# Performance work log

Measured on AMD Instinct MI355X. Metric: run time of the kernel, lower is better.

The kernel has to match this reference:

```python
import jax, jax.numpy as jnp
import numpy as np

D = 4          # simulated tensor-parallel devices (shard_axis size)
B, S = 2, 4096 # batch, seq_len
DIN_S = 512    # per-device input feature shard (full d_model = D*DIN_S = 2048)
DOUT_S = 2048  # per-device output feature shard (full d_out = D*DOUT_S = 8192)


def setup_inputs() -> dict:
    key = jax.random.key(0)
    kx, kw, kb = jax.random.split(key, 3)
    x = jax.random.normal(kx, (D, B, S, DIN_S), dtype=jnp.float32)
    # lecun_normal-style scale: std = 1/sqrt(fan_in) with fan_in = full input dim
    W = jax.random.normal(kw, (D, D, DIN_S, DOUT_S), dtype=jnp.float32) / np.sqrt(D * DIN_S)
    b = jax.random.normal(kb, (D, DOUT_S), dtype=jnp.float32) * 0.01
    return {"x": x, "W": W, "b": b}


def reference(x, W, b):
    # 'gather' TP strategy: device d gathers all input shards x_i and computes
    #   y_d = sum_i x_i @ W[d, i] + b[d]   (bias only added once, by shard idx==0)
    # x: [D, B, S, DIN_S], W: [D_out_dev, D_in_shard, DIN_S, DOUT_S], b: [D, DOUT_S]
    y = jnp.einsum('ibsk,diko->dbso', x, W)  # sum over gathered shards i and k
    return y + b[:, None, None, :]
```

## Files before the change

### kernel.cpp

```cpp
#include <hip/hip_runtime.h>
#include <hip/hip_bf16.h>

#define D_   4
#define M_   8192
#define K_   2048
#define N_   2048
#define DIN  512

typedef __attribute__((ext_vector_type(8))) short  short8v;
typedef __attribute__((ext_vector_type(4))) float  f32x4;

__device__ __forceinline__ unsigned short f2bf(float f) {
  union { float f; unsigned int u; } v; v.f = f;
  unsigned int u = v.u;
  return (unsigned short)((u + 0x7fffu + ((u >> 16) & 1u)) >> 16);
}

__global__ __launch_bounds__(256) void convert_x_kernel(const float* __restrict__ x,
                                                        unsigned short* __restrict__ A) {
  unsigned int tid = blockIdx.x * 256u + threadIdx.x;
  unsigned int kg  = tid & 63u;
  unsigned int i   = (tid >> 6) & 3u;
  unsigned int m   = tid >> 8;
  const float4* src = (const float4*)(x + (size_t)i * ((size_t)M_ * DIN)
                                        + (size_t)m * DIN + (size_t)kg * 8);
  float4 a = src[0];
  float4 b = src[1];
  uint4 pk;
  pk.x = (unsigned int)f2bf(a.x) | ((unsigned int)f2bf(a.y) << 16);
  pk.y = (unsigned int)f2bf(a.z) | ((unsigned int)f2bf(a.w) << 16);
  pk.z = (unsigned int)f2bf(b.x) | ((unsigned int)f2bf(b.y) << 16);
  pk.w = (unsigned int)f2bf(b.z) | ((unsigned int)f2bf(b.w) << 16);
  *(uint4*)(A + (size_t)tid * 8) = pk;
}

__global__ __launch_bounds__(256) void transpose_w_kernel(const float* __restrict__ W,
                                                          unsigned short* __restrict__ Wt) {
  __shared__ float tile[64][65];
  const int d  = blockIdx.z;
  const int k0 = blockIdx.x * 64;
  const int o0 = blockIdx.y * 64;
  const int t  = threadIdx.x;
  const float* src = W + (size_t)d * ((size_t)K_ * N_) + (size_t)k0 * N_ + o0;
  const int c4 = (t & 15) * 4;
  const int r  = t >> 4;
  #pragma unroll
  for (int j = 0; j < 64; j += 16) {
    float4 v = *(const float4*)(src + (size_t)(r + j) * N_ + c4);
    tile[r + j][c4 + 0] = v.x; tile[r + j][c4 + 1] = v.y;
    tile[r + j][c4 + 2] = v.z; tile[r + j][c4 + 3] = v.w;
  }
  __syncthreads();
  unsigned short* dst = Wt + (size_t)d * ((size_t)N_ * K_);
  const int kk = (t & 7) * 8;
  const int oo = t >> 3;
  #pragma unroll
  for (int p = 0; p < 64; p += 32) {
    const int o = oo + p;
    unsigned short tmp[8];
    #pragma unroll
    for (int i = 0; i < 8; i++) tmp[i] = f2bf(tile[kk + i][o]);
    *(uint4*)(dst + (size_t)(o0 + o) * K_ + k0 + kk) = *(uint4*)tmp;
  }
}

#define GLL16(gp, lp)                                                              \
  __builtin_amdgcn_global_load_lds(                                               \
      (const __attribute__((address_space(1))) void*)(gp),                        \
      (__attribute__((address_space(3))) void*)(lp), 16, 0, 0)

#define NT_ 64

__global__ __launch_bounds__(512, 2) void gemm_kernel(const unsigned short* __restrict__ A,
                                                      const unsigned short* __restrict__ Bt,
                                                      const float* __restrict__ bias,
                                                      float* __restrict__ C) {
  __shared__ __align__(16) unsigned short sT[4 * 16384];
  const int tid  = threadIdx.x;
  const int w    = tid >> 6;
  const int lane = tid & 63;
  const int d    = blockIdx.z;

  const int lin     = blockIdx.y * 8 + blockIdx.x;
  const int tile_id = (lin & 7) * 32 + (lin >> 3);
  const int tileM   = (tile_id >> 3) * 256;
  const int tileN   = (tile_id & 7) * 256;

  const unsigned short* Bd = Bt + (size_t)d * ((size_t)N_ * K_);

  const int lrow = lane >> 3;
  const int lc   = (lane & 7) ^ lrow;
  const int crow = w * 32 + lrow;
  const unsigned short* gS =
      (lc < 4) ? (A  + (size_t)(tileM + crow) * K_ + lc * 8)
               : (Bd + (size_t)(tileN + crow) * K_ + (lc - 4) * 8);
  unsigned short* lW = sT + w * 2048;

  const int wr = w >> 2;
  const int wc = w & 3;
  const int fr = lane & 15;
  const int qw = lane >> 4;
  const int xs = (qw ^ (fr & 7)) * 8;
  const int aoff = (wr * 128 + fr) * 64 + xs;
  const int boff = (wc *  64 + fr) * 64 + (xs ^ 32);

  f32x4 acc[8][4];
  #pragma unroll
  for (int mi = 0; mi < 8; ++mi)
    #pragma unroll
    for (int ni = 0; ni < 4; ++ni)
      acc[mi][ni] = (f32x4){0.f, 0.f, 0.f, 0.f};

#define ISSUE_TILE(tt) do {                                                   \
    unsigned short* lb_ = lW + ((tt) & 3) * 16384;                            \
    const size_t    ko_ = (size_t)(tt) * 32;                                  \
    GLL16(gS + ko_,                 lb_);                                     \
    GLL16(gS + ko_ + (size_t) 8*K_, lb_ +  512);                              \
    GLL16(gS + ko_ + (size_t)16*K_, lb_ + 1024);                              \
    GLL16(gS + ko_ + (size_t)24*K_, lb_ + 1536);                              \
  } while (0)

#define TILE_BODY(tt, WAITSTR, DOISSUE) do {                                  \
    asm volatile(WAITSTR ::: "memory");                                       \
    __builtin_amdgcn_s_barrier();                                             \
    __builtin_amdgcn_sched_barrier(0);                                        \
    if (DOISSUE) ISSUE_TILE((tt) + 3);                                        \
    const unsigned short* bT = sT + ((tt) & 3) * 16384;                       \
    short8v af[8], bfv[4];                                                    \
    _Pragma("unroll")                                                         \
    for (int mi = 0; mi < 8; ++mi) af[mi]  = *(const short8v*)(bT + aoff + mi * 1024); \
    _Pragma("unroll")                                                         \
    for (int ni = 0; ni < 4; ++ni) bfv[ni] = *(const short8v*)(bT + boff + ni * 1024); \
    __builtin_amdgcn_s_setprio(1);                                            \
    _Pragma("unroll")                                                         \
    for (int mi = 0; mi < 8; ++mi)                                            \
      _Pragma("unroll")                                                       \
      for (int ni = 0; ni < 4; ++ni)                                          \
        acc[mi][ni] = __builtin_amdgcn_mfma_f32_16x16x32_bf16(af[mi], bfv[ni],\
                                                              acc[mi][ni], 0, 0, 0); \
    __builtin_amdgcn_s_setprio(0);                                            \
  } while (0)

  ISSUE_TILE(0); ISSUE_TILE(1); ISSUE_TILE(2);

  for (int t = 0; t < NT_ - 2; ++t) {
    TILE_BODY(t, "s_waitcnt vmcnt(8)", t < NT_ - 3);
  }
  TILE_BODY(NT_ - 2, "s_waitcnt vmcnt(4)", false);
  TILE_BODY(NT_ - 1, "s_waitcnt vmcnt(0)", false);

#undef TILE_BODY
#undef ISSUE_TILE

  float* Cd       = C + (size_t)d * ((size_t)M_ * N_);
  const float* bd = bias + d * N_;
  #pragma unroll
  for (int ni = 0; ni < 4; ++ni) {
    const int col  = tileN + wc * 64 + ni * 16 + fr;
    const float bv = bd[col];
    #pragma unroll
    for (int mi = 0; mi < 8; ++mi) {
      const int row0 = tileM + wr * 128 + mi * 16 + qw * 4;
      #pragma unroll
      for (int r = 0; r < 4; ++r)
        Cd[(size_t)(row0 + r) * N_ + col] = acc[mi][ni][r] + bv;
    }
  }
}

__global__ void naive_kernel(const float* __restrict__ x, const float* __restrict__ W,
                             const float* __restrict__ bias, float* __restrict__ y) {
  long idx = (long)blockIdx.x * blockDim.x + threadIdx.x;
  if (idx >= (long)D_ * M_ * N_) return;
  int  n = (int)(idx % N_);
  long t = idx / N_;
  int  m = (int)(t % M_);
  int  d = (int)(t / M_);
  float acc = bias[d * N_ + n];
  const float* wd = W + (size_t)d * ((size_t)K_ * N_);
  for (int i = 0; i < D_; i++) {
    const float* xr = x + (size_t)i * ((size_t)M_ * DIN) + (size_t)m * DIN;
    const float* wr = wd + (size_t)i * ((size_t)DIN * N_) + n;
    #pragma unroll 4
    for (int k = 0; k < DIN; k++) acc += xr[k] * wr[(size_t)k * N_];
  }
  y[idx] = acc;
}

extern "C" void kernel_launch(void* const* d_in, const int* in_sizes, int n_in,
                              void* d_out, int out_size, void* d_ws, size_t ws_size,
                              hipStream_t stream) {
  const float* x    = (const float*)d_in[0];
  const float* W    = (const float*)d_in[1];
  const float* bias = (const float*)d_in[2];
  float* out        = (float*)d_out;

  const size_t a_elems  = (size_t)M_ * K_;
  const size_t wt_elems = (size_t)D_ * N_ * K_;
  const size_t need     = (a_elems + wt_elems) * sizeof(unsigned short);

  if (ws_size >= need) {
    unsigned short* Abf = (unsigned short*)d_ws;
    unsigned short* Wt  = Abf + a_elems;

    convert_x_kernel<<<(M_ * K_ / 8) / 256, 256, 0, stream>>>(x, Abf);

    dim3 tgrid(K_ / 64, N_ / 64, D_);
    transpose_w_kernel<<<tgrid, 256, 0, stream>>>(W, Wt);

    dim3 ggrid(N_ / 256, M_ / 256, D_);
    gemm_kernel<<<ggrid, 512, 0, stream>>>(Abf, Wt, bias, out);
  } else {
    long total = (long)D_ * M_ * N_;
    naive_kernel<<<(unsigned int)((total + 255) / 256), 256, 0, stream>>>(x, W, bias, out);
  }
}
```

Baseline: 588.4 us.

## Split GEMM k-tile into two half phases with interleaved loads and barriers

Restructures the main GEMM loop so each k-tile is processed in two halves of the M fragments. LDS fragment reads for the next half and half-sized global-to-LDS prefetches are issued between MFMA phases, separated by extra barriers, in a ping-pong style schedule. The aim is to overlap LDS reads and global loads with MFMA work and to cut register pressure from holding eight A fragments. The cost is more barriers per tile, and the reworked vmcnt wait accounting could stall or race if miscounted.

```diff
diff --git a/kernel.cpp b/kernel.cpp
--- a/kernel.cpp
+++ b/kernel.cpp
@@ -120,36 +120,68 @@
     GLL16(gS + ko_ + (size_t)24*K_, lb_ + 1536);                              \
   } while (0)
 
-#define TILE_BODY(tt, WAITSTR, DOISSUE) do {                                  \
-    asm volatile(WAITSTR ::: "memory");                                       \
-    __builtin_amdgcn_s_barrier();                                             \
-    __builtin_amdgcn_sched_barrier(0);                                        \
-    if (DOISSUE) ISSUE_TILE((tt) + 3);                                        \
+#define ISSUE_HALF(tt, jj) do {                                               \
+    unsigned short* lb_ = lW + ((tt) & 3) * 16384;                            \
+    const size_t    ko_ = (size_t)(tt) * 32;                                  \
+    GLL16(gS + ko_ + (size_t)(jj)     * 8 * K_, lb_ + (jj) * 512);            \
+    GLL16(gS + ko_ + (size_t)((jj)+1) * 8 * K_, lb_ + ((jj)+1) * 512);        \
+  } while (0)
+
+#define TILE_BODY(tt, ENDWAIT, DOISSUE) do {                                  \
     const unsigned short* bT = sT + ((tt) & 3) * 16384;                       \
-    short8v af[8], bfv[4];                                                    \
-    _Pragma("unroll")                                                         \
-    for (int mi = 0; mi < 8; ++mi) af[mi]  = *(const short8v*)(bT + aoff + mi * 1024); \
+    short8v afv[4], bfv[4];                                                   \
+                      \
+    _Pragma("unroll")                                                         \
+    for (int mi = 0; mi < 4; ++mi) afv[mi] = *(const short8v*)(bT + aoff + mi * 1024); \
     _Pragma("unroll")                                                         \
     for (int ni = 0; ni < 4; ++ni) bfv[ni] = *(const short8v*)(bT + boff + ni * 1024); \
+    if (DOISSUE) ISSUE_HALF((tt) + 3, 0);                                     \
+    __builtin_amdgcn_s_barrier();                                             \
+    asm volatile("s_waitcnt lgkmcnt(0)" ::: "memory");                        \
+    __builtin_amdgcn_sched_barrier(0);                                        \
     __builtin_amdgcn_s_setprio(1);                                            \
     _Pragma("unroll")                                                         \
-    for (int mi = 0; mi < 8; ++mi)                                            \
+    for (int mi = 0; mi < 4; ++mi)                                            \
       _Pragma("unroll")                                                       \
       for (int ni = 0; ni < 4; ++ni)                                          \
-        acc[mi][ni] = __builtin_amdgcn_mfma_f32_16x16x32_bf16(af[mi], bfv[ni],\
+        acc[mi][ni] = __builtin_amdgcn_mfma_f32_16x16x32_bf16(afv[mi], bfv[ni],\
                                                               acc[mi][ni], 0, 0, 0); \
     __builtin_amdgcn_s_setprio(0);                                            \
+    __builtin_amdgcn_sched_barrier(0);                                        \
+    __builtin_amdgcn_s_barrier();                                             \
+                    \
+    _Pragma("unroll")                                                         \
+    for (int mi = 0; mi < 4; ++mi) afv[mi] = *(const short8v*)(bT + aoff + (mi + 4) * 1024); \
+    if (DOISSUE) ISSUE_HALF((tt) + 3, 2);                                     \
+    __builtin_amdgcn_s_barrier();                                             \
+    asm volatile("s_waitcnt lgkmcnt(0)" ::: "memory");                        \
+    __builtin_amdgcn_sched_barrier(0);                                        \
+    __builtin_amdgcn_s_setprio(1);                                            \
+    _Pragma("unroll")                                                         \
+    for (int mi = 0; mi < 4; ++mi)                                            \
+      _Pragma("unroll")                                                       \
+      for (int ni = 0; ni < 4; ++ni)                                          \
+        acc[mi + 4][ni] = __builtin_amdgcn_mfma_f32_16x16x32_bf16(afv[mi], bfv[ni],\
+                                                                  acc[mi + 4][ni], 0, 0, 0); \
+    __builtin_amdgcn_s_setprio(0);                                            \
+    __builtin_amdgcn_sched_barrier(0);                                        \
+    asm volatile(ENDWAIT ::: "memory");                                       \
+    __builtin_amdgcn_s_barrier();                                             \
   } while (0)
 
   ISSUE_TILE(0); ISSUE_TILE(1); ISSUE_TILE(2);
-
-  for (int t = 0; t < NT_ - 2; ++t) {
-    TILE_BODY(t, "s_waitcnt vmcnt(8)", t < NT_ - 3);
-  }
-  TILE_BODY(NT_ - 2, "s_waitcnt vmcnt(4)", false);
-  TILE_BODY(NT_ - 1, "s_waitcnt vmcnt(0)", false);
+  asm volatile("s_waitcnt vmcnt(8)" ::: "memory");
+  __builtin_amdgcn_s_barrier();
+
+  for (int t = 0; t < NT_ - 3; ++t) {
+    TILE_BODY(t, "s_waitcnt vmcnt(8)", true);
+  }
+  TILE_BODY(NT_ - 3, "s_waitcnt vmcnt(4)", false);
+  TILE_BODY(NT_ - 2, "s_waitcnt vmcnt(0)", false);
+  TILE_BODY(NT_ - 1, "s_nop 0", false);
 
 #undef TILE_BODY
+#undef ISSUE_HALF
 #undef ISSUE_TILE
 
   float* Cd       = C + (size_t)d * ((size_t)M_ * N_);
```

Result: no change. 577.6 us (-1.8%).

## Retile GEMM to 128x256 tiles with 256 threads and 3-stage LDS pipeline

Applied to the files above, without the earlier changes.

Switches the bf16 MFMA GEMM from 256x256 tiles with 8 waves and a 4-deep LDS ring to 128x256 tiles with 4 waves, each computing a 64x128 sub-tile, and a 3-deep ring. The LDS layout changes to a new XOR swizzle that packs two rows per 64-element line. The raster swizzle of tile IDs is dropped, and the k-loop is unrolled by three to rotate the slots. The aim is less LDS per block and more blocks for better occupancy, at the cost of less A reuse per block and a shallower prefetch distance.

```diff
diff --git a/kernel.cpp b/kernel.cpp
--- a/kernel.cpp
+++ b/kernel.cpp
@@ -69,85 +69,89 @@
       (const __attribute__((address_space(1))) void*)(gp),                        \
       (__attribute__((address_space(3))) void*)(lp), 16, 0, 0)
 
-#define NT_ 64
-
-__global__ __launch_bounds__(512, 2) void gemm_kernel(const unsigned short* __restrict__ A,
+#define NT_    64
+#define SLOTE  12288
+
+__global__ __launch_bounds__(256, 2) void gemm_kernel(const unsigned short* __restrict__ A,
                                                       const unsigned short* __restrict__ Bt,
                                                       const float* __restrict__ bias,
                                                       float* __restrict__ C) {
-  __shared__ __align__(16) unsigned short sT[4 * 16384];
+  __shared__ __align__(16) unsigned short sT[3 * SLOTE];
   const int tid  = threadIdx.x;
   const int w    = tid >> 6;
   const int lane = tid & 63;
   const int d    = blockIdx.z;
-
-  const int lin     = blockIdx.y * 8 + blockIdx.x;
-  const int tile_id = (lin & 7) * 32 + (lin >> 3);
-  const int tileM   = (tile_id >> 3) * 256;
-  const int tileN   = (tile_id & 7) * 256;
+  const int tileN = blockIdx.x * 256;
+  const int tileM = blockIdx.y * 128;
 
   const unsigned short* Bd = Bt + (size_t)d * ((size_t)N_ * K_);
 
   const int lrow = lane >> 3;
-  const int lc   = (lane & 7) ^ lrow;
-  const int crow = w * 32 + lrow;
-  const unsigned short* gS =
-      (lc < 4) ? (A  + (size_t)(tileM + crow) * K_ + lc * 8)
-               : (Bd + (size_t)(tileN + crow) * K_ + (lc - 4) * 8);
-  unsigned short* lW = sT + w * 2048;
-
-  const int wr = w >> 2;
-  const int wc = w & 3;
+  const int sc   = (lane & 7) ^ lrow;
+  const int ch   = sc >> 2;
+  const int ck   = (sc & 3) * 8;
+  const unsigned short* src[6];
+  #pragma unroll
+  for (int g = 0; g < 6; ++g) {
+    const int gl = w * 6 + g;
+    src[g] = (gl < 8)
+        ? A  + (size_t)(tileM + gl * 16 + lrow * 2 + ch) * K_ + ck
+        : Bd + (size_t)(tileN + (gl - 8) * 16 + lrow * 2 + ch) * K_ + ck;
+  }
+  unsigned short* lW = sT + w * 3072;
+
+  const int wr = w >> 1;
+  const int wc = w & 1;
   const int fr = lane & 15;
   const int qw = lane >> 4;
-  const int xs = (qw ^ (fr & 7)) * 8;
-  const int aoff = (wr * 128 + fr) * 64 + xs;
-  const int boff = (wc *  64 + fr) * 64 + (xs ^ 32);
-
-  f32x4 acc[8][4];
-  #pragma unroll
-  for (int mi = 0; mi < 8; ++mi)
+  const int xoff = ((((fr & 1) * 4) + qw) ^ ((fr >> 1) & 7)) * 8;
+  const int aoff = wr * 2048 + (fr >> 1) * 64 + xoff;
+  const int boff = 4096 + wc * 4096 + (fr >> 1) * 64 + xoff;
+
+  f32x4 acc[4][8];
+  #pragma unroll
+  for (int mi = 0; mi < 4; ++mi)
     #pragma unroll
-    for (int ni = 0; ni < 4; ++ni)
+    for (int ni = 0; ni < 8; ++ni)
       acc[mi][ni] = (f32x4){0.f, 0.f, 0.f, 0.f};
 
-#define ISSUE_TILE(tt) do {                                                   \
-    unsigned short* lb_ = lW + ((tt) & 3) * 16384;                            \
+#define ISSUE_TILE(tt, ss) do {                                               \
+    unsigned short* lb_ = lW + (ss) * SLOTE;                                  \
     const size_t    ko_ = (size_t)(tt) * 32;                                  \
-    GLL16(gS + ko_,                 lb_);                                     \
-    GLL16(gS + ko_ + (size_t) 8*K_, lb_ +  512);                              \
-    GLL16(gS + ko_ + (size_t)16*K_, lb_ + 1024);                              \
-    GLL16(gS + ko_ + (size_t)24*K_, lb_ + 1536);                              \
+    GLL16(src[0] + ko_, lb_);        GLL16(src[1] + ko_, lb_ +  512);         \
+    GLL16(src[2] + ko_, lb_ + 1024); GLL16(src[3] + ko_, lb_ + 1536);         \
+    GLL16(src[4] + ko_, lb_ + 2048); GLL16(src[5] + ko_, lb_ + 2560);         \
   } while (0)
 
-#define TILE_BODY(tt, WAITSTR, DOISSUE) do {                                  \
+#define TILE_BODY(tt, ss, WAITSTR, DOISSUE, ss2) do {                         \
     asm volatile(WAITSTR ::: "memory");                                       \
     __builtin_amdgcn_s_barrier();                                             \
     __builtin_amdgcn_sched_barrier(0);                                        \
-    if (DOISSUE) ISSUE_TILE((tt) + 3);                                        \
-    const unsigned short* bT = sT + ((tt) & 3) * 16384;                       \
-    short8v af[8], bfv[4];                                                    \
+    if (DOISSUE) ISSUE_TILE((tt) + 2, ss2);                                   \
+    const unsigned short* bT = sT + (ss) * SLOTE;                             \
+    short8v af[4], bfv[8];                                                    \
     _Pragma("unroll")                                                         \
-    for (int mi = 0; mi < 8; ++mi) af[mi]  = *(const short8v*)(bT + aoff + mi * 1024); \
+    for (int mi = 0; mi < 4; ++mi) af[mi]  = *(const short8v*)(bT + aoff + mi * 512); \
     _Pragma("unroll")                                                         \
-    for (int ni = 0; ni < 4; ++ni) bfv[ni] = *(const short8v*)(bT + boff + ni * 1024); \
+    for (int ni = 0; ni < 8; ++ni) bfv[ni] = *(const short8v*)(bT + boff + ni * 512); \
     __builtin_amdgcn_s_setprio(1);                                            \
     _Pragma("unroll")                                                         \
-    for (int mi = 0; mi < 8; ++mi)                                            \
+    for (int mi = 0; mi < 4; ++mi)                                            \
       _Pragma("unroll")                                                       \
-      for (int ni = 0; ni < 4; ++ni)                                          \
+      for (int ni = 0; ni < 8; ++ni)                                          \
         acc[mi][ni] = __builtin_amdgcn_mfma_f32_16x16x32_bf16(af[mi], bfv[ni],\
                                                               acc[mi][ni], 0, 0, 0); \
     __builtin_amdgcn_s_setprio(0);                                            \
   } while (0)
 
-  ISSUE_TILE(0); ISSUE_TILE(1); ISSUE_TILE(2);
-
-  for (int t = 0; t < NT_ - 2; ++t) {
-    TILE_BODY(t, "s_waitcnt vmcnt(8)", t < NT_ - 3);
-  }
-  TILE_BODY(NT_ - 2, "s_waitcnt vmcnt(4)", false);
-  TILE_BODY(NT_ - 1, "s_waitcnt vmcnt(0)", false);
+  ISSUE_TILE(0, 0); ISSUE_TILE(1, 1);
+
+  for (int t3 = 0; t3 < NT_ - 1; t3 += 3) {
+    TILE_BODY(t3,     0, "s_waitcnt vmcnt(6)", true,              2);
+    TILE_BODY(t3 + 1, 1, "s_waitcnt vmcnt(6)", true,              0);
+    TILE_BODY(t3 + 2, 2, "s_waitcnt vmcnt(6)", (t3 + 4) < NT_,    1);
+  }
+  TILE_BODY(NT_ - 1, 0, "s_waitcnt vmcnt(0)", false, 0);
 
 #undef TILE_BODY
 #undef ISSUE_TILE
@@ -155,12 +159,12 @@
   float* Cd       = C + (size_t)d * ((size_t)M_ * N_);
   const float* bd = bias + d * N_;
   #pragma unroll
-  for (int ni = 0; ni < 4; ++ni) {
-    const int col  = tileN + wc * 64 + ni * 16 + fr;
+  for (int ni = 0; ni < 8; ++ni) {
+    const int col  = tileN + wc * 128 + ni * 16 + fr;
     const float bv = bd[col];
     #pragma unroll
-    for (int mi = 0; mi < 8; ++mi) {
-      const int row0 = tileM + wr * 128 + mi * 16 + qw * 4;
+    for (int mi = 0; mi < 4; ++mi) {
+      const int row0 = tileM + wr * 64 + mi * 16 + qw * 4;
       #pragma unroll
       for (int r = 0; r < 4; ++r)
         Cd[(size_t)(row0 + r) * N_ + col] = acc[mi][ni][r] + bv;
@@ -208,8 +212,8 @@
     dim3 tgrid(K_ / 64, N_ / 64, D_);
     transpose_w_kernel<<<tgrid, 256, 0, stream>>>(W, Wt);
 
-    dim3 ggrid(N_ / 256, M_ / 256, D_);
-    gemm_kernel<<<ggrid, 512, 0, stream>>>(Abf, Wt, bias, out);
+    dim3 ggrid(N_ / 256, M_ / 128, D_);
+    gemm_kernel<<<ggrid, 256, 0, stream>>>(Abf, Wt, bias, out);
   } else {
     long total = (long)D_ * M_ * N_;
     naive_kernel<<<(unsigned int)((total + 255) / 256), 256, 0, stream>>>(x, W, bias, out);
```

Measured after the change: 602.5 us. 1.02x slower.
